# Optimization experiments

Hardware: AMD Instinct MI355X
Metric: run time of the kernel (lower is better)

The kernel has to match this reference:

```python
import jax, jax.numpy as jnp
import numpy as np

# Fixed triangular structure: 19x19 -> 190 upper-triangular pairs
_IU, _JU = np.triu_indices(19)            # each (190,)
_FLAT = jnp.asarray(_IU * 19 + _JU)        # gather indices into the 361 axis
_IU = jnp.asarray(_IU)
_JU = jnp.asarray(_JU)
_H = 8                                      # num heads


def setup_inputs() -> dict:
    key = jax.random.key(0)
    ks = jax.random.split(key, 6)
    B, D = 4096, 64
    return {
        "x": jax.random.normal(ks[0], (B, 361, D), dtype=jnp.float32),
        "pos_emb": jax.random.normal(ks[1], (190, D), dtype=jnp.float32) * 0.1,
        "w_in": jax.random.normal(ks[2], (3 * D, D), dtype=jnp.float32) * 0.05,
        "b_in": jax.random.normal(ks[3], (3 * D,), dtype=jnp.float32) * 0.02,
        "w_out": jax.random.normal(ks[4], (D, D), dtype=jnp.float32) * 0.05,
        "b_out": jax.random.normal(ks[5], (D,), dtype=jnp.float32) * 0.02,
        "ln_g": jnp.ones((D,), dtype=jnp.float32),
        "ln_b": jnp.zeros((D,), dtype=jnp.float32),
    }


def _layer_norm(x, g, b, eps=1e-5):
    mu = jnp.mean(x, axis=-1, keepdims=True)
    var = jnp.mean(jnp.square(x - mu), axis=-1, keepdims=True)
    return (x - mu) * jax.lax.rsqrt(var + eps) * g + b


def reference(x, pos_emb, w_in, b_in, w_out, b_out, ln_g, ln_b):
    B, _, D = x.shape
    hd = D // _H  # head_dim = 8

    # --- gather 190 triangular positions out of 361 ---
    xt = x[:, _FLAT, :] + pos_emb                 # (B, 190, D)

    # --- MHA (eval mode, torch nn.MultiheadAttention semantics) ---
    qkv = jnp.einsum('bsd,ed->bse', xt, w_in) + b_in     # (B, 190, 3D)
    q, k, v = jnp.split(qkv, 3, axis=-1)
    def heads(t):
        return t.reshape(B, 190, _H, hd).transpose(0, 2, 1, 3)  # (B, H, S, hd)
    q, k, v = heads(q), heads(k), heads(v)
    scores = jnp.einsum('bhqd,bhkd->bhqk', q, k) / jnp.sqrt(jnp.float32(hd))
    attn = jax.nn.softmax(scores, axis=-1)
    o = jnp.einsum('bhqk,bhkd->bhqd', attn, v)           # (B, H, S, hd)
    o = o.transpose(0, 2, 1, 3).reshape(B, 190, D)
    attn_out = jnp.einsum('bsd,ed->bse', o, w_out) + b_out

    # --- residual + LayerNorm ---
    y = _layer_norm(attn_out + xt, ln_g, ln_b)           # (B, 190, D)

    # --- symmetric scatter back to 19x19 = 361 ---
    full = jnp.zeros((B, 19, 19, D), dtype=y.dtype)
    full = full.at[:, _IU, _JU, :].set(y)
    full = full.at[:, _JU, _IU, :].set(y)  # mirror; diagonal rewritten with same value
    return full.reshape(B, 361, D)
```

## Files before the change

kernel.cpp:

```cpp
#include <hip/hip_runtime.h>
#include <hip/hip_bf16.h>


typedef __bf16 bf8 __attribute__((ext_vector_type(8)));
typedef __bf16 bf2 __attribute__((ext_vector_type(2)));
typedef short s16x4 __attribute__((ext_vector_type(4)));
typedef float f32x4 __attribute__((ext_vector_type(4)));
typedef unsigned int u32x4 __attribute__((ext_vector_type(4)));
typedef unsigned int u32x2 __attribute__((ext_vector_type(2)));

#define LDS_BYTES 80960
#define OFF_XT 0
#define OFF_O  27360
#define OFF_VT 54720
#define OFF_TRI 80200
#define XS 72
#define OS 72
#define VS 196

__device__ __forceinline__ unsigned short f2b(float f) {
  __bf16 h = (__bf16)f;
  return __builtin_bit_cast(unsigned short, h);
}
__device__ __forceinline__ float b2f(unsigned short u) {
  unsigned int x = (unsigned int)u << 16;
  return __builtin_bit_cast(float, x);
}
__device__ __forceinline__ float b2f_lo(unsigned int u) {
  return __builtin_bit_cast(float, u << 16);
}
__device__ __forceinline__ float b2f_hi(unsigned int u) {
  return __builtin_bit_cast(float, u & 0xFFFF0000u);
}
__device__ __forceinline__ unsigned int pk(float lo, float hi) {
  bf2 v = { (__bf16)lo, (__bf16)hi };
  return __builtin_bit_cast(unsigned int, v);
}
__device__ __forceinline__ bf8 ldsb8(const unsigned short* p) {
  u32x4 u = *(const u32x4*)p;
  return __builtin_bit_cast(bf8, u);
}
__device__ __forceinline__ s16x4 as_bf4(u32x2 u) { return __builtin_bit_cast(s16x4, u); }
__device__ __forceinline__ f32x4 mfma16(bf8 a, bf8 b, f32x4 c) {
  return __builtin_amdgcn_mfma_f32_16x16x32_bf16(a, b, c, 0, 0, 0);
}
__device__ __forceinline__ f32x4 mfma16k(s16x4 a, s16x4 b, f32x4 c) {
  return __builtin_amdgcn_mfma_f32_16x16x16bf16_1k(a, b, c, 0, 0, 0);
}
__device__ __forceinline__ bf8 load_w8(const float* p) {
  float4 a = ((const float4*)p)[0];
  float4 b = ((const float4*)p)[1];
  u32x4 u = { pk(a.x, a.y), pk(a.z, a.w), pk(b.x, b.y), pk(b.z, b.w) };
  return __builtin_bit_cast(bf8, u);
}
__device__ __forceinline__ int tri_row(int s) {
  int i = (int)floorf((39.0f - sqrtf(1521.0f - 8.0f * (float)s)) * 0.5f);
  if (s < i * (39 - i) / 2) --i;
  else if (s >= (i + 1) * (38 - i) / 2) ++i;
  return i;
}

#define FOR12(M)  M(0) M(1) M(2) M(3) M(4) M(5) M(6) M(7) M(8) M(9) M(10) M(11)

__global__ void __launch_bounds__(512)
__attribute__((amdgpu_waves_per_eu(4, 4)))
tri_attn_kernel(const float* __restrict__ x, const float* __restrict__ pos,
                const float* __restrict__ w_in, const float* __restrict__ b_in,
                const float* __restrict__ w_out, const float* __restrict__ b_out,
                const float* __restrict__ ln_g, const float* __restrict__ ln_b,
                float* __restrict__ out)
{
  extern __shared__ char lds[];
  unsigned short* XT = (unsigned short*)(lds + OFF_XT);
  unsigned short* OB = (unsigned short*)(lds + OFF_O);
  unsigned short* VT = (unsigned short*)(lds + OFF_VT);
  unsigned int*  TRI = (unsigned int*)(lds + OFF_TRI);

  const int tid  = threadIdx.x;
  const int lane = tid & 63;
  const int wv   = tid >> 6;
  const int q15  = lane & 15;
  const int g    = lane >> 4;
  const int b    = blockIdx.x;
  const float qscale = 0.5100694858979282f;

  const float* xb = x + (size_t)b * (361 * 64);
  for (int idx = tid; idx < 3040; idx += 512) {
    int s = idx >> 4, c = idx & 15;
    int i = tri_row(s);
    int j = i + s - i * (39 - i) / 2;
    float4 v = ((const float4*)(xb + (i * 19 + j) * 64))[c];
    float4 p = ((const float4*)(pos + s * 64))[c];
    u32x2 wd = { pk(v.x + p.x, v.y + p.y), pk(v.z + p.z, v.w + p.w) };
    *(u32x2*)(XT + s * XS + c * 4) = wd;
    if (c == 0)
      TRI[s] = (unsigned int)(i * 19 + j) | ((unsigned int)(j * 19 + i) << 16);
  }
  if (tid < 64) *(unsigned int*)(VT + tid * VS + 190) = 0u;
  if (tid < 98) ((unsigned int*)(VT + 64 * VS))[tid] = 0x3F803F80u;
  __syncthreads();

  const int t   = wv >> 1;
  const int hh  = wv & 1;
  const int nt  = wv & 3;
  const int mtb = wv >> 2;
  const bool keep = ((g >> 1) == hh);

  #define DECL_K(I) u32x2 k##I;
  FOR12(DECL_K)

  {
    bf8 wq0 = load_w8(w_in + (nt * 16 + q15) * 64 + g * 8);
    bf8 wq1 = load_w8(w_in + (nt * 16 + q15) * 64 + 32 + g * 8);
    float bq = b_in[nt * 16 + q15];
    #pragma unroll
    for (int m6 = 0; m6 < 6; ++m6) {
      int mt = mtb + 2 * m6;
      f32x4 acc = {bq, bq, bq, bq};
      acc = mfma16(ldsb8(XT + (mt * 16 + q15) * XS + g * 8), wq0, acc);
      acc = mfma16(ldsb8(XT + (mt * 16 + q15) * XS + 32 + g * 8), wq1, acc);
      #pragma unroll
      for (int r = 0; r < 4; ++r) {
        int row = mt * 16 + g * 4 + r;
        if (row < 190) OB[row * OS + nt * 16 + q15] = f2b(acc[r] * qscale);
      }
    }
  }

  {
    bf8 wk0 = load_w8(w_in + (64 + t * 16 + q15) * 64 + g * 8);
    bf8 wk1 = load_w8(w_in + (64 + t * 16 + q15) * 64 + 32 + g * 8);
    float bk0 = b_in[64 + t * 16 + g * 4 + 0], bk1 = b_in[64 + t * 16 + g * 4 + 1];
    float bk2 = b_in[64 + t * 16 + g * 4 + 2], bk3 = b_in[64 + t * 16 + g * 4 + 3];
    #define KPROJ(I) { \
      f32x4 acc = {0.f, 0.f, 0.f, 0.f}; \
      acc = mfma16(wk0, ldsb8(XT + ((I) * 16 + q15) * XS + g * 8), acc); \
      acc = mfma16(wk1, ldsb8(XT + ((I) * 16 + q15) * XS + 32 + g * 8), acc); \
      k##I = u32x2{ pk(acc[0] + bk0, acc[1] + bk1), pk(acc[2] + bk2, acc[3] + bk3) }; }
    FOR12(KPROJ)
  }

  {
    bf8 wv0 = load_w8(w_in + (128 + nt * 16 + q15) * 64 + g * 8);
    bf8 wv1 = load_w8(w_in + (128 + nt * 16 + q15) * 64 + 32 + g * 8);
    float bv = b_in[128 + nt * 16 + q15];
    #pragma unroll
    for (int m6 = 0; m6 < 6; ++m6) {
      int mt = mtb + 2 * m6;
      f32x4 acc = {bv, bv, bv, bv};
      acc = mfma16(ldsb8(XT + (mt * 16 + q15) * XS + g * 8), wv0, acc);
      acc = mfma16(ldsb8(XT + (mt * 16 + q15) * XS + 32 + g * 8), wv1, acc);
      unsigned int w0 = pk(acc[0], acc[1]), w1 = pk(acc[2], acc[3]);
      unsigned short* dst = VT + (nt * 16 + q15) * VS + mt * 16 + g * 4;
      if (mt == 11 && g == 3) {
        *(unsigned int*)dst = w0;
      } else {
        u32x2 wd = {w0, w1};
        *(u32x2*)dst = wd;
      }
    }
  }
  __syncthreads();

  const int h = wv;
  const bool mk3 = (g == 3);
  const unsigned short* Vrow = VT + ((q15 < 8) ? (h * 8 + q15) : 64) * VS;

  #define DECL_V(I) u32x2 v##I;
  FOR12(DECL_V)
  #define VLOAD(I) v##I = *(const u32x2*)(Vrow + (I) * 16 + g * 4);
  FOR12(VLOAD)

  #define ATT_K(KT, OA) { \
    f32x4 sc = mfma16k(as_bf4(k##KT), qb4, f32x4{0.f, 0.f, 0.f, 0.f}); \
    float p0 = __builtin_amdgcn_exp2f(sc[0]); \
    float p1 = __builtin_amdgcn_exp2f(sc[1]); \
    float p2 = __builtin_amdgcn_exp2f(sc[2]); \
    float p3 = __builtin_amdgcn_exp2f(sc[3]); \
    if ((KT) == 11) { p2 = mk3 ? 0.f : p2; p3 = mk3 ? 0.f : p3; } \
    u32x2 pb = { pk(p0, p1), pk(p2, p3) }; \
    OA = mfma16k(as_bf4(v##KT), as_bf4(pb), OA); }

  #define ATT_MC(MC) { \
    u32x2 uq = *(const u32x2*)(OB + ((MC) * 16 + q15) * OS + t * 16 + g * 4); \
    u32x2 qb = { keep ? uq.x : 0u, keep ? uq.y : 0u }; \
    s16x4 qb4 = as_bf4(qb); \
    f32x4 o0 = {0.f, 0.f, 0.f, 0.f}, o1 = {0.f, 0.f, 0.f, 0.f}; \
    ATT_K(0, o0)  ATT_K(1, o1)  ATT_K(2, o0)  ATT_K(3, o1) \
    ATT_K(4, o0)  ATT_K(5, o1)  ATT_K(6, o0)  ATT_K(7, o1) \
    ATT_K(8, o0)  ATT_K(9, o1)  ATT_K(10, o0) ATT_K(11, o1) \
    f32x4 o = o0 + o1; \
    float Sv = __shfl(o[0], 32 + q15);         \
    float inv = __builtin_amdgcn_rcpf(Sv); \
    int qa = (MC) * 16 + q15; \
    if (g < 2 && qa < 190) { \
      u32x2 wd = { pk(o[0] * inv, o[1] * inv), pk(o[2] * inv, o[3] * inv) }; \
      *(u32x2*)(OB + qa * OS + h * 8 + g * 4) = wd; } }

  FOR12(ATT_MC)
  __syncthreads();

  {
    bf8 wo0 = load_w8(w_out + (nt * 16 + q15) * 64 + g * 8);
    bf8 wo1 = load_w8(w_out + (nt * 16 + q15) * 64 + 32 + g * 8);
    float bo = b_out[nt * 16 + q15];
    #pragma unroll
    for (int m6 = 0; m6 < 6; ++m6) {
      int mt = mtb + 2 * m6;
      f32x4 acc = {bo, bo, bo, bo};
      acc = mfma16(ldsb8(OB + (mt * 16 + q15) * OS + g * 8), wo0, acc);
      acc = mfma16(ldsb8(OB + (mt * 16 + q15) * OS + 32 + g * 8), wo1, acc);
      #pragma unroll
      for (int r = 0; r < 4; ++r) {
        int row = mt * 16 + g * 4 + r;
        if (row < 190) {
          int col = nt * 16 + q15;
          float z = acc[r] + b2f(XT[row * XS + col]);
          XT[row * XS + col] = f2b(z);
        }
      }
    }
  }
  __syncthreads();

  float* MU = (float*)(lds + OFF_VT);
  if (wv < 6) {
    const s16x4 ones4 = { (short)0x3F80, (short)0x3F80, (short)0x3F80, (short)0x3F80 };
    #pragma unroll
    for (int half = 0; half < 2; ++half) {
      int s0 = (wv + half * 6) * 16;
      f32x4 cs = {0.f, 0.f, 0.f, 0.f};
      f32x4 cq = {0.f, 0.f, 0.f, 0.f};
      #pragma unroll
      for (int c = 0; c < 4; ++c) {
        u32x2 zz = *(const u32x2*)(XT + (s0 + q15) * XS + c * 16 + g * 4);
        cs = mfma16k(as_bf4(zz), ones4, cs);
        float f0 = b2f_lo(zz.x), f1 = b2f_hi(zz.x);
        float f2 = b2f_lo(zz.y), f3 = b2f_hi(zz.y);
        u32x2 qq = { pk(f0 * f0, f1 * f1), pk(f2 * f2, f3 * f3) };
        cq = mfma16k(as_bf4(qq), ones4, cq);
      }
      if (q15 == 0) {
        #pragma unroll
        for (int r = 0; r < 4; ++r) {
          int row = s0 + g * 4 + r;
          if (row < 190) {
            float mu = cs[r] * 0.015625f;
            float var = cq[r] * 0.015625f - mu * mu;
            float2 mr = { mu, rsqrtf(var + 1e-5f) };
            *(float2*)(MU + row * 2) = mr;
          }
        }
      }
    }
  }
  __syncthreads();

  {
    float gg = ln_g[lane];
    float bb = ln_b[lane];
    float* outb = out + (size_t)b * (361 * 64);
    for (int s = wv; s < 190; s += 8) {
      float2 mr = *(const float2*)(MU + s * 2);
      unsigned int ij = TRI[s];
      float zv = b2f(XT[s * XS + lane]);
      float y = (zv - mr.x) * mr.y * gg + bb;
      outb[(ij & 0xFFFFu) * 64 + lane] = y;
      outb[(ij >> 16) * 64 + lane] = y;
    }
  }
}

extern "C" void kernel_launch(void* const* d_in, const int* in_sizes, int n_in,
                              void* d_out, int out_size, void* d_ws, size_t ws_size,
                              hipStream_t stream) {
  const float* x     = (const float*)d_in[0];
  const float* pos   = (const float*)d_in[1];
  const float* w_in  = (const float*)d_in[2];
  const float* b_in  = (const float*)d_in[3];
  const float* w_out = (const float*)d_in[4];
  const float* b_out = (const float*)d_in[5];
  const float* ln_g  = (const float*)d_in[6];
  const float* ln_b  = (const float*)d_in[7];
  float* out = (float*)d_out;
  (void)in_sizes; (void)n_in; (void)out_size; (void)d_ws; (void)ws_size;
  hipFuncSetAttribute((const void*)tri_attn_kernel,
                      hipFuncAttributeMaxDynamicSharedMemorySize, LDS_BYTES);
  tri_attn_kernel<<<4096, 512, LDS_BYTES, stream>>>(x, pos, w_in, b_in, w_out,
                                                    b_out, ln_g, ln_b, out);
}
```

Measured before the change: 264.9 us.

## Compute V per-head in registers, swizzle XT layout, raise occupancy target

Each wave now computes its own head's V tile directly into registers with MFMA, so the LDS VT buffer, its staging stores and the reload are gone. The ones row used for the softmax denominator is also produced in registers. XT switches from a padded stride-72 layout to an XOR-swizzled 64-wide layout to avoid bank conflicts. LDS shrinks from about 81KB to about 54KB and waves_per_eu is raised from 4 to 6 so more blocks can be resident. The cost is some redundant V projection work (half the lanes compute duplicate rows) and tighter register pressure from the higher occupancy cap.

```diff
diff --git a/kernel.cpp b/kernel.cpp
--- a/kernel.cpp
+++ b/kernel.cpp
@@ -9,14 +9,14 @@
 typedef unsigned int u32x4 __attribute__((ext_vector_type(4)));
 typedef unsigned int u32x2 __attribute__((ext_vector_type(2)));
 
-#define LDS_BYTES 80960
+#define LDS_BYTES 53960
 #define OFF_XT 0
-#define OFF_O  27360
-#define OFF_VT 54720
-#define OFF_TRI 80200
-#define XS 72
+#define OFF_O  24320
+#define OFF_MU 51680
+#define OFF_TRI 53200
 #define OS 72
-#define VS 196
+
+#define XTI(r, c) (((r) << 6) + (((c) ^ (((r) & 7) << 3))))
 
 __device__ __forceinline__ unsigned short f2b(float f) {
   __bf16 h = (__bf16)f;
@@ -63,7 +63,7 @@
 #define FOR12(M)  M(0) M(1) M(2) M(3) M(4) M(5) M(6) M(7) M(8) M(9) M(10) M(11)
 
 __global__ void __launch_bounds__(512)
-__attribute__((amdgpu_waves_per_eu(4, 4)))
+__attribute__((amdgpu_waves_per_eu(6, 6)))
 tri_attn_kernel(const float* __restrict__ x, const float* __restrict__ pos,
                 const float* __restrict__ w_in, const float* __restrict__ b_in,
                 const float* __restrict__ w_out, const float* __restrict__ b_out,
@@ -73,7 +73,7 @@
   extern __shared__ char lds[];
   unsigned short* XT = (unsigned short*)(lds + OFF_XT);
   unsigned short* OB = (unsigned short*)(lds + OFF_O);
-  unsigned short* VT = (unsigned short*)(lds + OFF_VT);
+  float*          MU = (float*)(lds + OFF_MU);
   unsigned int*  TRI = (unsigned int*)(lds + OFF_TRI);
 
   const int tid  = threadIdx.x;
@@ -82,6 +82,7 @@
   const int q15  = lane & 15;
   const int g    = lane >> 4;
   const int b    = blockIdx.x;
+  const int h    = wv;
   const float qscale = 0.5100694858979282f;
 
   const float* xb = x + (size_t)b * (361 * 64);
@@ -92,12 +93,10 @@
     float4 v = ((const float4*)(xb + (i * 19 + j) * 64))[c];
     float4 p = ((const float4*)(pos + s * 64))[c];
     u32x2 wd = { pk(v.x + p.x, v.y + p.y), pk(v.z + p.z, v.w + p.w) };
-    *(u32x2*)(XT + s * XS + c * 4) = wd;
+    *(u32x2*)(XT + XTI(s, c * 4)) = wd;
     if (c == 0)
       TRI[s] = (unsigned int)(i * 19 + j) | ((unsigned int)(j * 19 + i) << 16);
   }
-  if (tid < 64) *(unsigned int*)(VT + tid * VS + 190) = 0u;
-  if (tid < 98) ((unsigned int*)(VT + 64 * VS))[tid] = 0x3F803F80u;
   __syncthreads();
 
   const int t   = wv >> 1;
@@ -106,8 +105,8 @@
   const int mtb = wv >> 2;
   const bool keep = ((g >> 1) == hh);
 
-  #define DECL_K(I) u32x2 k##I;
-  FOR12(DECL_K)
+  #define DECL_KV(I) u32x2 k##I, v##I;
+  FOR12(DECL_KV)
 
   {
     bf8 wq0 = load_w8(w_in + (nt * 16 + q15) * 64 + g * 8);
@@ -117,8 +116,8 @@
     for (int m6 = 0; m6 < 6; ++m6) {
       int mt = mtb + 2 * m6;
       f32x4 acc = {bq, bq, bq, bq};
-      acc = mfma16(ldsb8(XT + (mt * 16 + q15) * XS + g * 8), wq0, acc);
-      acc = mfma16(ldsb8(XT + (mt * 16 + q15) * XS + 32 + g * 8), wq1, acc);
+      acc = mfma16(ldsb8(XT + XTI(mt * 16 + q15, g * 8)), wq0, acc);
+      acc = mfma16(ldsb8(XT + XTI(mt * 16 + q15, 32 + g * 8)), wq1, acc);
       #pragma unroll
       for (int r = 0; r < 4; ++r) {
         int row = mt * 16 + g * 4 + r;
@@ -134,42 +133,30 @@
     float bk2 = b_in[64 + t * 16 + g * 4 + 2], bk3 = b_in[64 + t * 16 + g * 4 + 3];
     #define KPROJ(I) { \
       f32x4 acc = {0.f, 0.f, 0.f, 0.f}; \
-      acc = mfma16(wk0, ldsb8(XT + ((I) * 16 + q15) * XS + g * 8), acc); \
-      acc = mfma16(wk1, ldsb8(XT + ((I) * 16 + q15) * XS + 32 + g * 8), acc); \
+      acc = mfma16(wk0, ldsb8(XT + XTI((I) * 16 + q15, g * 8)), acc); \
+      acc = mfma16(wk1, ldsb8(XT + XTI((I) * 16 + q15, 32 + g * 8)), acc); \
       k##I = u32x2{ pk(acc[0] + bk0, acc[1] + bk1), pk(acc[2] + bk2, acc[3] + bk3) }; }
     FOR12(KPROJ)
   }
 
   {
-    bf8 wv0 = load_w8(w_in + (128 + nt * 16 + q15) * 64 + g * 8);
-    bf8 wv1 = load_w8(w_in + (128 + nt * 16 + q15) * 64 + 32 + g * 8);
-    float bv = b_in[128 + nt * 16 + q15];
-    #pragma unroll
-    for (int m6 = 0; m6 < 6; ++m6) {
-      int mt = mtb + 2 * m6;
-      f32x4 acc = {bv, bv, bv, bv};
-      acc = mfma16(ldsb8(XT + (mt * 16 + q15) * XS + g * 8), wv0, acc);
-      acc = mfma16(ldsb8(XT + (mt * 16 + q15) * XS + 32 + g * 8), wv1, acc);
-      unsigned int w0 = pk(acc[0], acc[1]), w1 = pk(acc[2], acc[3]);
-      unsigned short* dst = VT + (nt * 16 + q15) * VS + mt * 16 + g * 4;
-      if (mt == 11 && g == 3) {
-        *(unsigned int*)dst = w0;
-      } else {
-        u32x2 wd = {w0, w1};
-        *(u32x2*)dst = wd;
-      }
-    }
-  }
-  __syncthreads();
-
-  const int h = wv;
+    bf8 wvb0 = load_w8(w_in + (128 + h * 8 + (q15 & 7)) * 64 + g * 8);
+    bf8 wvb1 = load_w8(w_in + (128 + h * 8 + (q15 & 7)) * 64 + 32 + g * 8);
+    float bv = b_in[128 + h * 8 + (q15 & 7)];
+    const unsigned int ONE2 = 0x3F803F80u;
+    #define VPROJ(I) { \
+      f32x4 acc = {bv, bv, bv, bv}; \
+      acc = mfma16(ldsb8(XT + XTI((I) * 16 + q15, g * 8)), wvb0, acc); \
+      acc = mfma16(ldsb8(XT + XTI((I) * 16 + q15, 32 + g * 8)), wvb1, acc); \
+      unsigned int lo = pk(acc[0], acc[1]); \
+      unsigned int hi = pk(acc[2], acc[3]); \
+      if ((I) == 11) hi = (g == 3) ? 0u : hi;     \
+      v##I = (q15 < 8) ? u32x2{lo, hi} : u32x2{ONE2, ONE2}; }
+    FOR12(VPROJ)
+  }
+  __syncthreads();
+
   const bool mk3 = (g == 3);
-  const unsigned short* Vrow = VT + ((q15 < 8) ? (h * 8 + q15) : 64) * VS;
-
-  #define DECL_V(I) u32x2 v##I;
-  FOR12(DECL_V)
-  #define VLOAD(I) v##I = *(const u32x2*)(Vrow + (I) * 16 + g * 4);
-  FOR12(VLOAD)
 
   #define ATT_K(KT, OA) { \
     f32x4 sc = mfma16k(as_bf4(k##KT), qb4, f32x4{0.f, 0.f, 0.f, 0.f}); \
@@ -215,15 +202,14 @@
         int row = mt * 16 + g * 4 + r;
         if (row < 190) {
           int col = nt * 16 + q15;
-          float z = acc[r] + b2f(XT[row * XS + col]);
-          XT[row * XS + col] = f2b(z);
+          float z = acc[r] + b2f(XT[XTI(row, col)]);
+          XT[XTI(row, col)] = f2b(z);
         }
       }
     }
   }
   __syncthreads();
 
-  float* MU = (float*)(lds + OFF_VT);
   if (wv < 6) {
     const s16x4 ones4 = { (short)0x3F80, (short)0x3F80, (short)0x3F80, (short)0x3F80 };
     #pragma unroll
@@ -233,7 +219,7 @@
       f32x4 cq = {0.f, 0.f, 0.f, 0.f};
       #pragma unroll
       for (int c = 0; c < 4; ++c) {
-        u32x2 zz = *(const u32x2*)(XT + (s0 + q15) * XS + c * 16 + g * 4);
+        u32x2 zz = *(const u32x2*)(XT + XTI(s0 + q15, c * 16 + g * 4));
         cs = mfma16k(as_bf4(zz), ones4, cs);
         float f0 = b2f_lo(zz.x), f1 = b2f_hi(zz.x);
         float f2 = b2f_lo(zz.y), f3 = b2f_hi(zz.y);
@@ -263,7 +249,7 @@
     for (int s = wv; s < 190; s += 8) {
       float2 mr = *(const float2*)(MU + s * 2);
       unsigned int ij = TRI[s];
-      float zv = b2f(XT[s * XS + lane]);
+      float zv = b2f(XT[XTI(s, lane)]);
       float y = (zv - mr.x) * mr.y * gg + bb;
       outb[(ij & 0xFFFFu) * 64 + lane] = y;
       outb[(ij >> 16) * 64 + lane] = y;
```

After: 752.1 us. 184% more time.
